# Performance work log

Measured on AMD Instinct MI355X. Metric: run time of the kernel, lower is better.

The kernel has to match this reference:

```python
import jax, jax.numpy as jnp
import numpy as np

# Multi-scale feature pyramid (H, W) per level, standard Deformable-DETR for ~800x800 input
SHAPES = [(100, 100), (50, 50), (25, 25), (13, 13)]
D = 256      # d_model
NH = 8       # n_heads
NL = 4       # n_levels
NP = 4       # n_points
HD = D // NH # head_dim = 32
B = 2
S = sum(h * w for h, w in SHAPES)  # 13294
Lq = S  # encoder-style: one query per multi-scale token


def setup_inputs() -> dict:
    key = jax.random.key(0)
    ks = jax.random.split(key, 11)
    return {
        "query": jax.random.normal(ks[0], (B, Lq, D), jnp.float32),
        "reference_points": jax.random.uniform(ks[1], (B, Lq, NL, 2), jnp.float32),
        "value": jax.random.normal(ks[2], (B, S, D), jnp.float32),
        "W_val": jax.random.normal(ks[3], (D, D), jnp.float32) * 0.02,
        "b_val": jnp.zeros((D,), jnp.float32),
        "W_off": jax.random.normal(ks[4], (D, NH * NL * NP * 2), jnp.float32) * 0.01,
        "b_off": jax.random.normal(ks[5], (NH * NL * NP * 2,), jnp.float32) * 0.5,
        "W_attn": jax.random.normal(ks[6], (D, NH * NL * NP), jnp.float32) * 0.02,
        "b_attn": jnp.zeros((NH * NL * NP,), jnp.float32),
        "W_out": jax.random.normal(ks[7], (D, D), jnp.float32) * 0.02,
        "b_out": jnp.zeros((D,), jnp.float32),
    }


def _bilinear_sample(valf, x, y, H, W):
    """grid_sample(mode=bilinear, padding_mode=zeros, align_corners=False).
    valf: [N, H*W, C] flattened feature map; x, y: [N, P] pixel-space coords
    (already converted via x = loc_x*W - 0.5). Returns [N, P, C].
    """
    x0 = jnp.floor(x); y0 = jnp.floor(y)
    x1 = x0 + 1.0;     y1 = y0 + 1.0
    wx1 = x - x0; wx0 = 1.0 - wx1
    wy1 = y - y0; wy0 = 1.0 - wy1

    def corner(xi, yi, w):
        inb = (xi >= 0) & (xi <= W - 1) & (yi >= 0) & (yi <= H - 1)
        xi_c = jnp.clip(xi, 0, W - 1).astype(jnp.int32)
        yi_c = jnp.clip(yi, 0, H - 1).astype(jnp.int32)
        idx = yi_c * W + xi_c                                   # [N, P]
        v = jnp.take_along_axis(valf, idx[..., None], axis=1)   # [N, P, C]
        return v * (w * inb.astype(valf.dtype))[..., None]

    return (corner(x0, y0, wx0 * wy0) + corner(x1, y0, wx1 * wy0)
            + corner(x0, y1, wx0 * wy1) + corner(x1, y1, wx1 * wy1))


def reference(query, reference_points, value, W_val, b_val, W_off, b_off,
              W_attn, b_attn, W_out, b_out):
    Bq, L, _ = query.shape
    # value projection, split into heads: [B, S, NH, HD]
    val = (value @ W_val + b_val).reshape(Bq, S, NH, HD)
    # sampling offsets and attention weights from query
    offsets = (query @ W_off + b_off).reshape(Bq, L, NH, NL, NP, 2)
    w = (query @ W_attn + b_attn).reshape(Bq, L, NH, NL * NP)
    w = jax.nn.softmax(w, axis=-1).reshape(Bq, L, NH, NL, NP)
    # normalize offsets by (W, H) per level; 2D reference points path
    offset_norm = jnp.array([[wd, h] for h, wd in SHAPES], jnp.float32)  # [NL, 2]
    locs = (reference_points[:, :, None, :, None, :]
            + offsets / offset_norm[None, None, None, :, None, :])       # [B,L,NH,NL,NP,2]

    splits = [h * wd for h, wd in SHAPES]
    starts = np.concatenate([[0], np.cumsum(splits)])
    out_acc = jnp.zeros((Bq, L, NH, HD), query.dtype)
    for lvl, (H, W) in enumerate(SHAPES):
        vl = val[:, starts[lvl]:starts[lvl + 1]]                 # [B, HW, NH, HD]
        vl = vl.transpose(0, 2, 1, 3).reshape(Bq * NH, H * W, HD)
        loc = locs[:, :, :, lvl].transpose(0, 2, 1, 3, 4).reshape(Bq * NH, L * NP, 2)
        x = loc[..., 0] * W - 0.5   # align_corners=False pixel coords
        y = loc[..., 1] * H - 0.5
        s = _bilinear_sample(vl, x, y, H, W).reshape(Bq, NH, L, NP, HD)
        wl = w[:, :, :, lvl].transpose(0, 2, 1, 3)               # [B, NH, L, NP]
        out_acc = out_acc + jnp.einsum('bhqpd,bhqp->bqhd', s, wl)
    out = out_acc.reshape(Bq, L, NH * HD)
    return out @ W_out + b_out
```

## Files before the change

kernel.cpp:

```cpp
#include <hip/hip_runtime.h>
#include <hip/hip_bf16.h>
#include <math.h>

#define B_    2
#define NH_   8
#define NL_   4
#define NP_   4
#define HD_   32
#define S_    13294
#define L_    13294
#define M_    26588

__device__ __constant__ int c_H[NL_]     = {100, 50, 25, 13};
__device__ __constant__ int c_W[NL_]     = {100, 50, 25, 13};
__device__ __constant__ int c_start[NL_] = {0, 10000, 12500, 13125};

typedef __attribute__((ext_vector_type(8))) _Float16 f16x8;
typedef __attribute__((ext_vector_type(2))) _Float16 f16x2;
typedef __attribute__((ext_vector_type(4))) float    float4v;

__device__ __forceinline__ unsigned short f2h(float f) {
    _Float16 h = (_Float16)f;
    return __builtin_bit_cast(unsigned short, h);
}
__device__ __forceinline__ float h2f(unsigned short u) {
    _Float16 h = __builtin_bit_cast(_Float16, u);
    return (float)h;
}
__device__ __forceinline__ f16x2 pkrtz(float a, float b) {
    return __builtin_bit_cast(f16x2, __builtin_amdgcn_cvt_pkrtz(a, b));
}

__global__ __launch_bounds__(256) void prep_weights(
    const float* __restrict__ W_val, const float* __restrict__ W_off,
    const float* __restrict__ W_attn, const float* __restrict__ b_off,
    const float* __restrict__ b_attn, const float* __restrict__ W_out,
    unsigned short* __restrict__ wt_val, unsigned short* __restrict__ wt_oa,
    unsigned short* __restrict__ wt_out, float* __restrict__ bias_oa)
{
    int i = blockIdx.x * 256 + threadIdx.x;
    if (i < 65536) {
        int n = i >> 8, k = i & 255;
        wt_val[i] = f2h(W_val[k * 256 + n]);
    } else if (i < 65536 + 98304) {
        int j = i - 65536;
        int n = j >> 8, k = j & 255;
        float v = (n < 256) ? W_off[k * 256 + n] : W_attn[k * 128 + (n - 256)];
        wt_oa[j] = f2h(v);
    } else if (i < 65536 + 98304 + 65536) {
        int j = i - 163840;
        int n = j >> 8, k = j & 255;
        wt_out[j] = f2h(W_out[k * 256 + n]);
    } else if (i < 229376 + 384) {
        int j = i - 229376;
        bias_oa[j] = (j < 256) ? b_off[j] : b_attn[j - 256];
    }
}

template<int NT, int OUT, bool AF32>
__device__ __forceinline__ void gemm_body(
    const void* __restrict__ Av,
    const unsigned short* __restrict__ WT,
    const float* __restrict__ bias,
    void* __restrict__ Cv,
    unsigned short (* __restrict__ As)[64][40],
    int colBase)
{
    const int tid  = threadIdx.x;
    const int lane = tid & 63;
    const int wave = tid >> 6;
    const int rowBase = blockIdx.x * 64;
    const int wcol = colBase + wave * (NT * 16);

    const int ar   = tid >> 2;
    const int ako  = (tid & 3) * 8;
    const int grow = rowBase + ar;
    const int fr   = lane & 15;
    const int fk   = (lane >> 4) * 8;

    float4v acc[4][NT] = {};

    const unsigned short* bbase[NT];
#pragma unroll
    for (int t = 0; t < NT; ++t)
        bbase[t] = WT + (size_t)(wcol + t * 16 + fr) * 256 + fk;

    f16x8 curB[NT], nxtB[NT];
    float4 ra0, ra1;
    f16x8  rah;

    auto loadA = [&](int k0) {
        if constexpr (AF32) {
            const float* A = (const float*)Av;
            if (grow < M_) {
                ra0 = *reinterpret_cast<const float4*>(A + (size_t)grow * 256 + k0 + ako);
                ra1 = *reinterpret_cast<const float4*>(A + (size_t)grow * 256 + k0 + ako + 4);
            } else { ra0 = make_float4(0.f,0.f,0.f,0.f); ra1 = ra0; }
        } else {
            const unsigned short* A = (const unsigned short*)Av;
            if (grow < M_)
                rah = *reinterpret_cast<const f16x8*>(A + (size_t)grow * 256 + k0 + ako);
            else
                rah = f16x8{};
        }
    };
    auto storeA = [&](int buf) {
        f16x8 s;
        if constexpr (AF32) {
            f16x2 p0 = pkrtz(ra0.x, ra0.y);
            f16x2 p1 = pkrtz(ra0.z, ra0.w);
            f16x2 p2 = pkrtz(ra1.x, ra1.y);
            f16x2 p3 = pkrtz(ra1.z, ra1.w);
            s[0]=p0[0]; s[1]=p0[1]; s[2]=p1[0]; s[3]=p1[1];
            s[4]=p2[0]; s[5]=p2[1]; s[6]=p3[0]; s[7]=p3[1];
        } else {
            s = rah;
        }
        *reinterpret_cast<f16x8*>(&As[buf][ar][ako]) = s;
    };
    auto loadB = [&](f16x8* dst, int k0) {
#pragma unroll
        for (int t = 0; t < NT; ++t)
            dst[t] = *reinterpret_cast<const f16x8*>(bbase[t] + k0);
    };

    loadA(0);
    loadB(curB, 0);
    storeA(0);
    loadA(32);

#pragma unroll
    for (int it = 0; it < 8; ++it) {
        __syncthreads();
        f16x8 af[4];
#pragma unroll
        for (int t = 0; t < 4; ++t)
            af[t] = *reinterpret_cast<const f16x8*>(&As[it & 1][t * 16 + fr][fk]);
        if (it < 7) {
            storeA((it + 1) & 1);
            if (it < 6) loadA((it + 2) * 32);
            loadB(nxtB, (it + 1) * 32);
        }
#pragma unroll
        for (int mt = 0; mt < 4; ++mt)
#pragma unroll
            for (int nt = 0; nt < NT; ++nt)
                acc[mt][nt] = __builtin_amdgcn_mfma_f32_16x16x32_f16(
                    af[mt], curB[nt], acc[mt][nt], 0, 0, 0);
        if (it < 7) {
#pragma unroll
            for (int t = 0; t < NT; ++t) curB[t] = nxtB[t];
        }
    }

    const int dn  = lane & 15;
    const int dm0 = (lane >> 4) * 4;
#pragma unroll
    for (int mt = 0; mt < 4; ++mt) {
#pragma unroll
        for (int nt = 0; nt < NT; ++nt) {
            const int col = wcol + nt * 16 + dn;
            const float bv = bias[col];
#pragma unroll
            for (int r = 0; r < 4; ++r) {
                const int row = rowBase + mt * 16 + dm0 + r;
                if (row < M_) {
                    const float v = acc[mt][nt][r] + bv;
                    if constexpr (OUT == 0)
                        ((unsigned short*)Cv)[(size_t)row * 256 + col] = f2h(v);
                    else if constexpr (OUT == 1)
                        ((unsigned short*)Cv)[(size_t)row * 384 + col] = f2h(v);
                    else
                        ((float*)Cv)[(size_t)row * 256 + col] = v;
                }
            }
        }
    }
}

__global__ __launch_bounds__(256) void gemm_vq(
    const float* __restrict__ value, const float* __restrict__ query,
    const unsigned short* __restrict__ wt_val, const unsigned short* __restrict__ wt_oa,
    const float* __restrict__ b_val, const float* __restrict__ bias_oa,
    unsigned short* __restrict__ val_f16, unsigned short* __restrict__ oa_f16)
{
    __shared__ unsigned short As[2][64][40];
    if (blockIdx.y == 0)
        gemm_body<4, 0, true>(value, wt_val, b_val, val_f16, As, 0);
    else if (blockIdx.y == 1)
        gemm_body<3, 1, true>(query, wt_oa, bias_oa, oa_f16, As, 0);
    else
        gemm_body<3, 1, true>(query, wt_oa, bias_oa, oa_f16, As, 192);
}

__global__ __launch_bounds__(256) void gemm_out3(
    const unsigned short* __restrict__ Af16,
    const unsigned short* __restrict__ WT,
    const float* __restrict__ bias, float* __restrict__ C)
{
    __shared__ unsigned short As[2][64][40];
    gemm_body<4, 2, false>(Af16, WT, bias, C, As, 0);
}

__global__ __launch_bounds__(256, 8) void deform_sample_v6(
    const unsigned short* __restrict__ val,
    const float* __restrict__ refp,
    const unsigned short* __restrict__ oa,
    unsigned short* __restrict__ acc)
{
    __shared__ int sP[4][1088];

    const int tid  = threadIdx.x;
    const int wave = tid >> 6;
    const int l    = tid & 63;

    const int q   = l >> 5;
    const int h   = (l >> 2) & 7;
    const int lvl = l & 3;
    const int qw  = blockIdx.x * 8 + wave * 2 + q;
    const int bq  = min(qw, M_ - 1);

    int* __restrict__ sw = sP[wave];

    {
        const int2 lgi = *reinterpret_cast<const int2*>(
            oa + (size_t)bq * 384 + 256 + h * 16 + lvl * 4);
        const f16x2 lp0 = __builtin_bit_cast(f16x2, lgi.x);
        const f16x2 lp1 = __builtin_bit_cast(f16x2, lgi.y);
        float lg[4] = { (float)lp0[0], (float)lp0[1], (float)lp1[0], (float)lp1[1] };

        float m = fmaxf(fmaxf(lg[0], lg[1]), fmaxf(lg[2], lg[3]));
        m = fmaxf(m, __shfl_xor(m, 1));
        m = fmaxf(m, __shfl_xor(m, 2));

        float e[4], s = 0.f;
#pragma unroll
        for (int j = 0; j < 4; ++j) { e[j] = __expf(lg[j] - m); s += e[j]; }
        s += __shfl_xor(s, 1);
        s += __shfl_xor(s, 2);
        const float rinv = 1.f / s;

        const int Wi = c_W[lvl], Hi = c_H[lvl], st = c_start[lvl];
        const float2 rxy = *reinterpret_cast<const float2*>(
            refp + ((size_t)bq * NL_ + lvl) * 2);
        const f16x8 off8 = *reinterpret_cast<const f16x8*>(
            oa + (size_t)bq * 384 + h * 32 + lvl * 8);

#pragma unroll
        for (int j = 0; j < 4; ++j) {
            const float wgt = e[j] * rinv;
            const float x = rxy.x * (float)Wi + (float)off8[2 * j]     - 0.5f;
            const float y = rxy.y * (float)Hi + (float)off8[2 * j + 1] - 0.5f;
            const float x0f = floorf(x), y0f = floorf(y);
            const int   x0 = (int)x0f,   y0 = (int)y0f;
            const float wx1 = x - x0f, wx0 = 1.f - wx1;
            const float wy1 = y - y0f, wy0 = 1.f - wy1;

            const int   cx[4] = {x0, x0 + 1, x0,     x0 + 1};
            const int   cy[4] = {y0, y0,     y0 + 1, y0 + 1};
            const float cw[4] = {wx0 * wy0, wx1 * wy0, wx0 * wy1, wx1 * wy1};
            const int base = q * 544 + (lvl * 4 + j) * 34 + h;
#pragma unroll
            for (int c = 0; c < 4; ++c) {
                const bool inb = (cx[c] >= 0) & (cx[c] < Wi) & (cy[c] >= 0) & (cy[c] < Hi);
                const int xi = min(max(cx[c], 0), Wi - 1);
                const int yi = min(max(cy[c], 0), Hi - 1);
                const int idx = st + yi * Wi + xi;
                const unsigned short wh = f2h(inb ? wgt * cw[c] : 0.f);
                sw[base + c * 8] = idx | ((int)wh << 16);
            }
        }
    }

    const int d4 = lvl;
    const unsigned short* vb = val + (size_t)(bq / L_) * S_ * 256 + h * 32 + d4 * 8;
    const int rbase = q * 544 + h;

    f16x2 A0{}, A1{}, A2{}, A3{};
#pragma unroll 8
    for (int i = 0; i < 64; ++i) {
        const int lp = i >> 2;
        const int c  = i & 3;
        const int pk = sw[rbase + lp * 34 + c * 8];
        const unsigned wb = (unsigned)pk >> 16;
        const f16x2 w2 = __builtin_bit_cast(f16x2, (wb << 16) | wb);
        const int4 u = *reinterpret_cast<const int4*>(
            vb + (size_t)((unsigned)pk & 0xffffu) * 256);
        A0 += w2 * __builtin_bit_cast(f16x2, u.x);
        A1 += w2 * __builtin_bit_cast(f16x2, u.y);
        A2 += w2 * __builtin_bit_cast(f16x2, u.z);
        A3 += w2 * __builtin_bit_cast(f16x2, u.w);
    }
    if (qw < M_) {
        int4 o;
        o.x = __builtin_bit_cast(int, A0);
        o.y = __builtin_bit_cast(int, A1);
        o.z = __builtin_bit_cast(int, A2);
        o.w = __builtin_bit_cast(int, A3);
        *reinterpret_cast<int4*>(acc + (size_t)qw * 256 + h * 32 + d4 * 8) = o;
    }
}

extern "C" void kernel_launch(void* const* d_in, const int* in_sizes, int n_in,
                              void* d_out, int out_size, void* d_ws, size_t ws_size,
                              hipStream_t stream) {
    const float* query  = (const float*)d_in[0];
    const float* refp   = (const float*)d_in[1];
    const float* value  = (const float*)d_in[2];
    const float* W_val  = (const float*)d_in[3];
    const float* b_val  = (const float*)d_in[4];
    const float* W_off  = (const float*)d_in[5];
    const float* b_off  = (const float*)d_in[6];
    const float* W_attn = (const float*)d_in[7];
    const float* b_attn = (const float*)d_in[8];
    const float* W_out  = (const float*)d_in[9];
    const float* b_out  = (const float*)d_in[10];
    float* out = (float*)d_out;

    char* ws = (char*)d_ws;
    const size_t mb = (size_t)M_ * 256;
    unsigned short* val_f16 = (unsigned short*)ws;  ws += mb * 2;
    unsigned short* acc_f16 = (unsigned short*)ws;  ws += mb * 2;
    unsigned short* oa_f16  = (unsigned short*)ws;  ws += (size_t)M_ * 384 * 2;
    unsigned short* wt_val  = (unsigned short*)ws;  ws += 65536 * 2;
    unsigned short* wt_oa   = (unsigned short*)ws;  ws += 98304 * 2;
    unsigned short* wt_out  = (unsigned short*)ws;  ws += 65536 * 2;
    float*          bias_oa = (float*)ws;           ws += 384 * 4;

    dim3 blk(256);

    prep_weights<<<dim3(898), blk, 0, stream>>>(
        W_val, W_off, W_attn, b_off, b_attn, W_out, wt_val, wt_oa, wt_out, bias_oa);

    gemm_vq<<<dim3((M_ + 63) / 64, 3), blk, 0, stream>>>(
        value, query, wt_val, wt_oa, b_val, bias_oa, val_f16, oa_f16);

    deform_sample_v6<<<dim3((M_ + 7) / 8), blk, 0, stream>>>(val_f16, refp, oa_f16, acc_f16);

    gemm_out3<<<dim3((M_ + 63) / 64), blk, 0, stream>>>(acc_f16, wt_out, b_out, out);
}
```

Before: 206.8 us.

## Retile GEMMs so each wave owns its own row strip and removes block barriers

The GEMM body moves from a 64-row block tile with columns split across waves to a 128-row by 64-column block tile. Each wave now loads and owns its own 32-row A strip in private LDS, so the per-iteration __syncthreads is dropped. The grid grows along y to cover the output columns, which means the A rows are re-read once per column block (4x for the value and output GEMMs, 6x for query). The intent is to remove barrier stalls and raise parallelism. The cost is more global A traffic and fewer MFMAs per A fragment.

```diff
diff --git a/kernel.cpp b/kernel.cpp
--- a/kernel.cpp
+++ b/kernel.cpp
@@ -58,65 +58,72 @@
 }
 
 template<int NT, int OUT, bool AF32>
-__device__ __forceinline__ void gemm_body(
+__device__ __forceinline__ void gemm_wv(
     const void* __restrict__ Av,
     const unsigned short* __restrict__ WT,
     const float* __restrict__ bias,
     void* __restrict__ Cv,
-    unsigned short (* __restrict__ As)[64][40],
+    unsigned short (* __restrict__ sA)[2][32][40],
     int colBase)
 {
     const int tid  = threadIdx.x;
     const int lane = tid & 63;
     const int wave = tid >> 6;
-    const int rowBase = blockIdx.x * 64;
-    const int wcol = colBase + wave * (NT * 16);
-
-    const int ar   = tid >> 2;
-    const int ako  = (tid & 3) * 8;
-    const int grow = rowBase + ar;
-    const int fr   = lane & 15;
-    const int fk   = (lane >> 4) * 8;
-
-    float4v acc[4][NT] = {};
+    const int rowBase = blockIdx.x * 128 + wave * 32;
+
+    const int ar  = lane >> 2;
+    const int ako = (lane & 3) * 8;
+    const int fr  = lane & 15;
+    const int fk  = (lane >> 4) * 8;
+
+    float4v acc[2][NT] = {};
 
     const unsigned short* bbase[NT];
 #pragma unroll
     for (int t = 0; t < NT; ++t)
-        bbase[t] = WT + (size_t)(wcol + t * 16 + fr) * 256 + fk;
+        bbase[t] = WT + (size_t)(colBase + t * 16 + fr) * 256 + fk;
 
     f16x8 curB[NT], nxtB[NT];
-    float4 ra0, ra1;
-    f16x8  rah;
+    float4 ra0, ra1, rb0, rb1;
+    f16x8  rah_a, rah_b;
 
     auto loadA = [&](int k0) {
+        const int r0 = rowBase + ar;
+        const int r1 = rowBase + 16 + ar;
         if constexpr (AF32) {
             const float* A = (const float*)Av;
-            if (grow < M_) {
-                ra0 = *reinterpret_cast<const float4*>(A + (size_t)grow * 256 + k0 + ako);
-                ra1 = *reinterpret_cast<const float4*>(A + (size_t)grow * 256 + k0 + ako + 4);
+            if (r0 < M_) {
+                ra0 = *reinterpret_cast<const float4*>(A + (size_t)r0 * 256 + k0 + ako);
+                ra1 = *reinterpret_cast<const float4*>(A + (size_t)r0 * 256 + k0 + ako + 4);
             } else { ra0 = make_float4(0.f,0.f,0.f,0.f); ra1 = ra0; }
+            if (r1 < M_) {
+                rb0 = *reinterpret_cast<const float4*>(A + (size_t)r1 * 256 + k0 + ako);
+                rb1 = *reinterpret_cast<const float4*>(A + (size_t)r1 * 256 + k0 + ako + 4);
+            } else { rb0 = make_float4(0.f,0.f,0.f,0.f); rb1 = rb0; }
         } else {
             const unsigned short* A = (const unsigned short*)Av;
-            if (grow < M_)
-                rah = *reinterpret_cast<const f16x8*>(A + (size_t)grow * 256 + k0 + ako);
-            else
-                rah = f16x8{};
-        }
+            rah_a = (r0 < M_) ? *reinterpret_cast<const f16x8*>(A + (size_t)r0 * 256 + k0 + ako)
+                              : f16x8{};
+            rah_b = (r1 < M_) ? *reinterpret_cast<const f16x8*>(A + (size_t)r1 * 256 + k0 + ako)
+                              : f16x8{};
+        }
+    };
+    auto packA = [&](const float4& u0, const float4& u1) -> f16x8 {
+        const f16x2 p0 = pkrtz(u0.x, u0.y);
+        const f16x2 p1 = pkrtz(u0.z, u0.w);
+        const f16x2 p2 = pkrtz(u1.x, u1.y);
+        const f16x2 p3 = pkrtz(u1.z, u1.w);
+        f16x8 s;
+        s[0]=p0[0]; s[1]=p0[1]; s[2]=p1[0]; s[3]=p1[1];
+        s[4]=p2[0]; s[5]=p2[1]; s[6]=p3[0]; s[7]=p3[1];
+        return s;
     };
     auto storeA = [&](int buf) {
-        f16x8 s;
-        if constexpr (AF32) {
-            f16x2 p0 = pkrtz(ra0.x, ra0.y);
-            f16x2 p1 = pkrtz(ra0.z, ra0.w);
-            f16x2 p2 = pkrtz(ra1.x, ra1.y);
-            f16x2 p3 = pkrtz(ra1.z, ra1.w);
-            s[0]=p0[0]; s[1]=p0[1]; s[2]=p1[0]; s[3]=p1[1];
-            s[4]=p2[0]; s[5]=p2[1]; s[6]=p3[0]; s[7]=p3[1];
-        } else {
-            s = rah;
-        }
-        *reinterpret_cast<f16x8*>(&As[buf][ar][ako]) = s;
+        f16x8 sa, sb;
+        if constexpr (AF32) { sa = packA(ra0, ra1); sb = packA(rb0, rb1); }
+        else                { sa = rah_a;           sb = rah_b;           }
+        *reinterpret_cast<f16x8*>(&sA[wave][buf][ar][ako])      = sa;
+        *reinterpret_cast<f16x8*>(&sA[wave][buf][16 + ar][ako]) = sb;
     };
     auto loadB = [&](f16x8* dst, int k0) {
 #pragma unroll
@@ -131,22 +138,21 @@
 
 #pragma unroll
     for (int it = 0; it < 8; ++it) {
-        __syncthreads();
-        f16x8 af[4];
-#pragma unroll
-        for (int t = 0; t < 4; ++t)
-            af[t] = *reinterpret_cast<const f16x8*>(&As[it & 1][t * 16 + fr][fk]);
+        f16x8 af0 = *reinterpret_cast<const f16x8*>(&sA[wave][it & 1][fr][fk]);
+        f16x8 af1 = *reinterpret_cast<const f16x8*>(&sA[wave][it & 1][16 + fr][fk]);
         if (it < 7) {
             storeA((it + 1) & 1);
             if (it < 6) loadA((it + 2) * 32);
             loadB(nxtB, (it + 1) * 32);
         }
 #pragma unroll
-        for (int mt = 0; mt < 4; ++mt)
-#pragma unroll
-            for (int nt = 0; nt < NT; ++nt)
-                acc[mt][nt] = __builtin_amdgcn_mfma_f32_16x16x32_f16(
-                    af[mt], curB[nt], acc[mt][nt], 0, 0, 0);
+        for (int nt = 0; nt < NT; ++nt)
+            acc[0][nt] = __builtin_amdgcn_mfma_f32_16x16x32_f16(
+                af0, curB[nt], acc[0][nt], 0, 0, 0);
+#pragma unroll
+        for (int nt = 0; nt < NT; ++nt)
+            acc[1][nt] = __builtin_amdgcn_mfma_f32_16x16x32_f16(
+                af1, curB[nt], acc[1][nt], 0, 0, 0);
         if (it < 7) {
 #pragma unroll
             for (int t = 0; t < NT; ++t) curB[t] = nxtB[t];
@@ -156,10 +162,10 @@
     const int dn  = lane & 15;
     const int dm0 = (lane >> 4) * 4;
 #pragma unroll
-    for (int mt = 0; mt < 4; ++mt) {
+    for (int mt = 0; mt < 2; ++mt) {
 #pragma unroll
         for (int nt = 0; nt < NT; ++nt) {
-            const int col = wcol + nt * 16 + dn;
+            const int col = colBase + nt * 16 + dn;
             const float bv = bias[col];
 #pragma unroll
             for (int r = 0; r < 4; ++r) {
@@ -184,13 +190,12 @@
     const float* __restrict__ b_val, const float* __restrict__ bias_oa,
     unsigned short* __restrict__ val_f16, unsigned short* __restrict__ oa_f16)
 {
-    __shared__ unsigned short As[2][64][40];
-    if (blockIdx.y == 0)
-        gemm_body<4, 0, true>(value, wt_val, b_val, val_f16, As, 0);
-    else if (blockIdx.y == 1)
-        gemm_body<3, 1, true>(query, wt_oa, bias_oa, oa_f16, As, 0);
+    __shared__ unsigned short sA[4][2][32][40];
+    const int y = blockIdx.y;
+    if (y < 4)
+        gemm_wv<4, 0, true>(value, wt_val, b_val, val_f16, sA, y * 64);
     else
-        gemm_body<3, 1, true>(query, wt_oa, bias_oa, oa_f16, As, 192);
+        gemm_wv<4, 1, true>(query, wt_oa, bias_oa, oa_f16, sA, (y - 4) * 64);
 }
 
 __global__ __launch_bounds__(256) void gemm_out3(
@@ -198,8 +203,8 @@
     const unsigned short* __restrict__ WT,
     const float* __restrict__ bias, float* __restrict__ C)
 {
-    __shared__ unsigned short As[2][64][40];
-    gemm_body<4, 2, false>(Af16, WT, bias, C, As, 0);
+    __shared__ unsigned short sA[4][2][32][40];
+    gemm_wv<4, 2, false>(Af16, WT, bias, C, sA, blockIdx.y * 64);
 }
 
 __global__ __launch_bounds__(256, 8) void deform_sample_v6(
@@ -328,14 +333,15 @@
     float*          bias_oa = (float*)ws;           ws += 384 * 4;
 
     dim3 blk(256);
+    const int rb = (M_ + 127) / 128;
 
     prep_weights<<<dim3(898), blk, 0, stream>>>(
         W_val, W_off, W_attn, b_off, b_attn, W_out, wt_val, wt_oa, wt_out, bias_oa);
 
-    gemm_vq<<<dim3((M_ + 63) / 64, 3), blk, 0, stream>>>(
+    gemm_vq<<<dim3(rb, 10), blk, 0, stream>>>(
         value, query, wt_val, wt_oa, b_val, bias_oa, val_f16, oa_f16);
 
     deform_sample_v6<<<dim3((M_ + 7) / 8), blk, 0, stream>>>(val_f16, refp, oa_f16, acc_f16);
 
-    gemm_out3<<<dim3((M_ + 63) / 64), blk, 0, stream>>>(acc_f16, wt_out, b_out, out);
-}
+    gemm_out3<<<dim3(rb, 4), blk, 0, stream>>>(acc_f16, wt_out, b_out, out);
+}
```

New measurement: 226.5 us. +9.5%, slower.
